# Optimization experiments

Measured on AMD Instinct MI355X. Metric: run time of the kernel, lower is better.

The kernel has to match this reference:

```python
import jax, jax.numpy as jnp
import numpy as np

B, L, V, H = 2, 2048, 1024, 16
HD = V // H  # head size 64
EPS = 1e-3   # keras LayerNormalization default


def setup_inputs() -> dict:
    key = jax.random.key(0)
    ks = jax.random.split(key, 10)
    scale = 1.0 / np.sqrt(V)
    return {
        "query": jax.random.normal(ks[0], (B, L, V), jnp.float32),
        "key_t": jax.random.normal(ks[1], (B, L, V), jnp.float32),
        "value": jax.random.normal(ks[2], (B, L, V), jnp.float32),
        "Wq": jax.random.normal(ks[3], (H, V, HD), jnp.float32) * scale,
        "Wk": jax.random.normal(ks[4], (H, V, HD), jnp.float32) * scale,
        "Wv": jax.random.normal(ks[5], (H, V, HD), jnp.float32) * scale,
        "gamma": jnp.ones((V,), jnp.float32),
        "beta": jnp.zeros((V,), jnp.float32),
        "query_mask": jax.random.randint(ks[6], (B, L), 0, 2, jnp.int32),
        "value_mask": jax.random.randint(ks[7], (B, L), 0, 2, jnp.int32),
    }


def reference(query, key_t, value, Wq, Wk, Wv, gamma, beta, query_mask, value_mask):
    qm = query_mask.astype(jnp.float32)  # (B,L)
    vm = value_mask.astype(jnp.float32)  # (B,L)

    # per-head no-bias Dense projections, batched over heads
    Q = jnp.einsum('blv,hvd->bhld', query, Wq)
    K = jnp.einsum('blv,hvd->bhld', key_t, Wk)
    Vh = jnp.einsum('blv,hvd->bhld', value, Wv)

    scores = jnp.einsum('bhld,bhmd->bhlm', Q, K) / jnp.sqrt(jnp.float32(HD))
    attn = jax.nn.softmax(scores, axis=-1)

    # post-softmax multiplicative masking (faithful to original)
    tri = jnp.tril(jnp.ones((L, L), jnp.float32))  # (L,L) causal
    attn = attn * tri[None, None, :, :]
    attn = attn * qm[:, None, :, None] * vm[:, None, None, :]

    heads = jnp.einsum('bhlm,bhmd->bhld', attn, Vh)
    x = heads.transpose(0, 2, 1, 3).reshape(B, L, V)  # concat heads

    # dropout is identity at inference
    y = x + query
    mu = jnp.mean(y, axis=-1, keepdims=True)
    var = jnp.mean((y - mu) ** 2, axis=-1, keepdims=True)
    return gamma * (y - mu) * jax.lax.rsqrt(var + EPS) + beta
```

## Files before the change

kernel.cpp:

```cpp
#include <hip/hip_runtime.h>
#include <math.h>

constexpr int NB = 2;
constexpr int SL = 2048;
constexpr int NV = 1024;
constexpr int NH = 16;
constexpr int DH = 64;
constexpr float LN_EPS = 1e-3f;

typedef __bf16 bf16_t;
typedef __bf16 v8bf __attribute__((ext_vector_type(8)));
typedef float  v4f  __attribute__((ext_vector_type(4)));

__device__ __forceinline__ unsigned pack_bf16(float a, float b) {
  unsigned short ua = __builtin_bit_cast(unsigned short, (bf16_t)a);
  unsigned short ub = __builtin_bit_cast(unsigned short, (bf16_t)b);
  return (unsigned)ua | ((unsigned)ub << 16);
}
__device__ __forceinline__ void async_cp16(const void* g, void* l) {
  __builtin_amdgcn_global_load_lds(
      (const __attribute__((address_space(1))) unsigned int*)g,
      (__attribute__((address_space(3))) unsigned int*)l, 16, 0, 0);
}

__global__ __launch_bounds__(256)
void wcvt(const float* __restrict__ Wq, const float* __restrict__ Wk,
          const float* __restrict__ Wv, bf16_t* __restrict__ Wt) {
  __shared__ float ls[64][65];
  const int z = blockIdx.z;
  const float* W = z == 0 ? Wq : (z == 1 ? Wk : Wv);
  const float sc = z == 0 ? 0.125f * 1.44269504f : 1.0f;
  const int h = blockIdx.y, v0 = blockIdx.x * 64;
  const int t = threadIdx.x;
  const int rr = t >> 4, c4 = t & 15;
  const float* src = W + ((size_t)h * NV + v0) * DH;
#pragma unroll
  for (int it = 0; it < 4; ++it) {
    float4 f = *(const float4*)(src + (size_t)(rr + it * 16) * DH + c4 * 4);
    ls[rr + it * 16][c4 * 4 + 0] = f.x;
    ls[rr + it * 16][c4 * 4 + 1] = f.y;
    ls[rr + it * 16][c4 * 4 + 2] = f.z;
    ls[rr + it * 16][c4 * 4 + 3] = f.w;
  }
  __syncthreads();
  const int dd = t >> 2, vq = t & 3;
  bf16_t tmp[16];
#pragma unroll
  for (int i = 0; i < 16; ++i) tmp[i] = (bf16_t)(ls[vq * 16 + i][dd] * sc);
  bf16_t* dst = Wt + ((size_t)z * NV + h * 64 + dd) * NV + v0 + vq * 16;
  *(v8bf*)dst = *(v8bf*)&tmp[0];
  *(v8bf*)(dst + 8) = *(v8bf*)&tmp[8];
}

__global__ __launch_bounds__(256, 3)
void proj_mfma(const float* __restrict__ A0, const float* __restrict__ A1,
               const float* __restrict__ A2, const bf16_t* __restrict__ Wtb,
               const int* __restrict__ vmask,
               bf16_t* __restrict__ O0, bf16_t* __restrict__ O1,
               bf16_t* __restrict__ O2) {
  __shared__ __align__(16) bf16_t Asb[2][128 * 40];
  __shared__ __align__(16) bf16_t Wsb[2][128 * 32];

  const int id = blockIdx.x;
  const int z = id >> 8;
  const int m0 = (id & 31) * 128;
  const int n0 = ((id >> 5) & 7) * 128;
  const float*  A   = z == 0 ? A0 : (z == 1 ? A1 : A2);
  bf16_t*       out = z == 0 ? O0 : (z == 1 ? O1 : O2);
  const bf16_t* W   = Wtb + (size_t)z * NV * NV;

  const int t = threadIdx.x, w = t >> 6, lane = t & 63;
  const int g = lane >> 4, lx = lane & 15;
  const int rbase = (w >> 1) * 64, cbase = (w & 1) * 64;

  const int ar_r = t >> 1;
  const int ar_h = (t & 1) * 16;
  float4 ar[4];
  auto gloadA = [&](int k0) {
#pragma unroll
    for (int s = 0; s < 4; ++s)
      ar[s] = *(const float4*)(A + (size_t)(m0 + ar_r) * NV + k0 + ar_h + s * 4);
  };
  auto writeA = [&](int buf) {
    const int c0 = (ar_h >> 3);
    uint4 u0 = {pack_bf16(ar[0].x, ar[0].y), pack_bf16(ar[0].z, ar[0].w),
                pack_bf16(ar[1].x, ar[1].y), pack_bf16(ar[1].z, ar[1].w)};
    uint4 u1 = {pack_bf16(ar[2].x, ar[2].y), pack_bf16(ar[2].z, ar[2].w),
                pack_bf16(ar[3].x, ar[3].y), pack_bf16(ar[3].z, ar[3].w)};
    *(uint4*)((char*)Asb[buf] + ar_r * 80 + (c0 + 0) * 16) = u0;
    *(uint4*)((char*)Asb[buf] + ar_r * 80 + (c0 + 1) * 16) = u1;
  };
  auto stageW = [&](int k0, int buf) {
#pragma unroll
    for (int s = 0; s < 2; ++s) {
      const int r = w * 32 + s * 16 + (lane >> 2);
      const int c = (lane & 3) ^ (r & 3);
      async_cp16(W + (size_t)(n0 + r) * NV + k0 + c * 8,
                 (char*)Wsb[buf] + (w * 32 + s * 16) * 64);
    }
  };

  v4f acc[4][4] = {};

  gloadA(0);
  stageW(0, 0);
  writeA(0);
  __syncthreads();

  for (int it = 0; it < 32; ++it) {
    const int buf = it & 1;
    if (it < 31) { gloadA((it + 1) * 32); stageW((it + 1) * 32, buf ^ 1); }
    v8bf af[4], wf[4];
#pragma unroll
    for (int rt = 0; rt < 4; ++rt) {
      const int row = rbase + rt * 16 + lx;
      af[rt] = *(const v8bf*)((const char*)Asb[buf] + row * 80 + g * 16);
    }
#pragma unroll
    for (int ct = 0; ct < 4; ++ct) {
      const int row = cbase + ct * 16 + lx;
      wf[ct] = *(const v8bf*)((const char*)Wsb[buf] + row * 64 +
                              ((g ^ (row & 3)) * 16));
    }
#pragma unroll
    for (int rt = 0; rt < 4; ++rt)
#pragma unroll
      for (int ct = 0; ct < 4; ++ct)
        acc[rt][ct] = __builtin_amdgcn_mfma_f32_16x16x32_bf16(
            af[rt], wf[ct], acc[rt][ct], 0, 0, 0);
    if (it < 31) { writeA(buf ^ 1); __syncthreads(); }
  }

  if (z < 2) {
#pragma unroll
    for (int rt = 0; rt < 4; ++rt) {
#pragma unroll
      for (int reg = 0; reg < 4; ++reg) {
        const int row = m0 + rbase + rt * 16 + g * 4 + reg;
        const int b = row >> 11, l = row & (SL - 1);
#pragma unroll
        for (int ct = 0; ct < 4; ++ct) {
          const int n = n0 + cbase + ct * 16 + lx;
          const int h = n >> 6, d = n & 63;
          out[((size_t)(b * NH + h) * SL + l) * DH + d] = (bf16_t)acc[rt][ct][reg];
        }
      }
    }
  } else {
#pragma unroll
    for (int rt = 0; rt < 4; ++rt) {
      const int row = m0 + rbase + rt * 16 + g * 4;
      const int b = row >> 11, l = row & (SL - 1);
      float vm0 = (float)vmask[b * SL + l + 0];
      float vm1 = (float)vmask[b * SL + l + 1];
      float vm2 = (float)vmask[b * SL + l + 2];
      float vm3 = (float)vmask[b * SL + l + 3];
#pragma unroll
      for (int ct = 0; ct < 4; ++ct) {
        const int n = n0 + cbase + ct * 16 + lx;
        const int h = n >> 6, d = n & 63;
        uint2 u = {pack_bf16(acc[rt][ct][0] * vm0, acc[rt][ct][1] * vm1),
                   pack_bf16(acc[rt][ct][2] * vm2, acc[rt][ct][3] * vm3)};
        *(uint2*)&out[((size_t)(b * NH + h) * DH + d) * SL + l] = u;
      }
    }
  }
}

__global__ __launch_bounds__(256, 3)
void attn_mfma(const bf16_t* __restrict__ Qg, const bf16_t* __restrict__ Kg,
               const bf16_t* __restrict__ Vtg_all, const int* __restrict__ qmask,
               float* __restrict__ Xout) {
  __shared__ __align__(16) bf16_t kbuf[2][64 * 64];
  __shared__ __align__(16) bf16_t vbuf[2][64 * 64];
  __shared__ __align__(16) bf16_t Ps[4][32][72];

  const int id = blockIdx.x;
  const int bh = (id & 7) | ((id >> 7) << 3);
  const int qb = 15 - ((id >> 3) & 15);
  const int t = threadIdx.x, w = t >> 6, lane = t & 63;
  const int g = lane >> 4, lx = lane & 15;
  const int b = bh >> 4, h = bh & 15;
  const int l0 = qb * 128;
  const int lastAct = 2 * qb + 1;

  const bf16_t* Kb  = Kg + (size_t)bh * SL * DH;
  const bf16_t* Vtg = Vtg_all + (size_t)bh * DH * SL;

  v8bf qf[2][2];
#pragma unroll
  for (int qt = 0; qt < 2; ++qt)
#pragma unroll
    for (int ks = 0; ks < 2; ++ks)
      qf[qt][ks] = *(const v8bf*)&Qg[((size_t)bh * SL + l0 + w * 32 + qt * 16 + lx) * DH +
                                     ks * 32 + g * 8];

  v4f O[2][4] = {};
  float suml[2] = {0.f, 0.f};

  const int sr_off = lane >> 3, sc_l = lane & 7;
  auto stageK = [&](int mb, int buf) {
#pragma unroll
    for (int s = 0; s < 2; ++s) {
      const int r = w * 16 + s * 8 + sr_off;
      const int c = sc_l ^ (r & 7);
      async_cp16(Kb + (size_t)(mb + r) * DH + c * 8,
                 (char*)kbuf[buf] + (w * 16 + s * 8) * 128);
    }
  };
  auto stageV = [&](int mb, int buf) {
#pragma unroll
    for (int s = 0; s < 2; ++s) {
      const int r = w * 16 + s * 8 + sr_off;
      const int c = sc_l ^ (r & 7);
      async_cp16(Vtg + (size_t)r * SL + mb + c * 8,
                 (char*)vbuf[buf] + (w * 16 + s * 8) * 128);
    }
  };

  stageK(0, 0);
  stageV(0, 0);

  for (int mt = 0; mt <= lastAct; ++mt) {
    const int pb = mt & 1;
    __syncthreads();
    if (mt < SL / 64 - 1)  stageK((mt + 1) * 64, pb ^ 1);
    if (mt + 1 <= lastAct) stageV((mt + 1) * 64, pb ^ 1);

    v4f S[4][2];
#pragma unroll
    for (int mt2 = 0; mt2 < 4; ++mt2) {
      S[mt2][0] = (v4f){0.f, 0.f, 0.f, 0.f};
      S[mt2][1] = (v4f){0.f, 0.f, 0.f, 0.f};
    }
#pragma unroll
    for (int ks = 0; ks < 2; ++ks)
#pragma unroll
      for (int mt2 = 0; mt2 < 4; ++mt2) {
        const int row = mt2 * 16 + lx;
        v8bf kf = *(const v8bf*)((const char*)kbuf[pb] + row * 128 +
                                 (((ks * 4 + g) ^ (lx & 7)) * 16));
#pragma unroll
        for (int qt = 0; qt < 2; ++qt)
          S[mt2][qt] = __builtin_amdgcn_mfma_f32_16x16x32_bf16(
              kf, qf[qt][ks], S[mt2][qt], 0, 0, 0);
      }

    const bool diagzone = (mt >= 2 * qb);
#pragma unroll
    for (int mt2 = 0; mt2 < 4; ++mt2)
#pragma unroll
      for (int qt = 0; qt < 2; ++qt) {
        float e0 = __builtin_amdgcn_exp2f(S[mt2][qt][0]);
        float e1 = __builtin_amdgcn_exp2f(S[mt2][qt][1]);
        float e2 = __builtin_amdgcn_exp2f(S[mt2][qt][2]);
        float e3 = __builtin_amdgcn_exp2f(S[mt2][qt][3]);
        suml[qt] += (e0 + e1) + (e2 + e3);
        if (diagzone) {
          const int ml = mt * 64 + mt2 * 16 + g * 4;
          const int ql = l0 + w * 32 + qt * 16 + lx;
          e0 = (ml + 0 <= ql) ? e0 : 0.f;
          e1 = (ml + 1 <= ql) ? e1 : 0.f;
          e2 = (ml + 2 <= ql) ? e2 : 0.f;
          e3 = (ml + 3 <= ql) ? e3 : 0.f;
        }
        uint2 u = {pack_bf16(e0, e1), pack_bf16(e2, e3)};
        *(uint2*)&Ps[w][qt * 16 + lx][mt2 * 16 + g * 4] = u;
      }

#pragma unroll
    for (int ks = 0; ks < 2; ++ks) {
      v8bf pf[2];
#pragma unroll
      for (int qt = 0; qt < 2; ++qt)
        pf[qt] = *(const v8bf*)&Ps[w][qt * 16 + lx][ks * 32 + g * 8];
#pragma unroll
      for (int dt = 0; dt < 4; ++dt) {
        const int row = dt * 16 + lx;
        v8bf vf = *(const v8bf*)((const char*)vbuf[pb] + row * 128 +
                                 (((ks * 4 + g) ^ (lx & 7)) * 16));
#pragma unroll
        for (int qt = 0; qt < 2; ++qt)
          O[qt][dt] = __builtin_amdgcn_mfma_f32_16x16x32_bf16(
              pf[qt], vf, O[qt][dt], 0, 0, 0);
      }
    }
  }

  for (int mt = lastAct + 1; mt < SL / 64; ++mt) {
    const int pb = mt & 1;
    __syncthreads();
    if (mt < SL / 64 - 1) stageK((mt + 1) * 64, pb ^ 1);
    v4f S[4][2];
#pragma unroll
    for (int mt2 = 0; mt2 < 4; ++mt2) {
      S[mt2][0] = (v4f){0.f, 0.f, 0.f, 0.f};
      S[mt2][1] = (v4f){0.f, 0.f, 0.f, 0.f};
    }
#pragma unroll
    for (int ks = 0; ks < 2; ++ks)
#pragma unroll
      for (int mt2 = 0; mt2 < 4; ++mt2) {
        const int row = mt2 * 16 + lx;
        v8bf kf = *(const v8bf*)((const char*)kbuf[pb] + row * 128 +
                                 (((ks * 4 + g) ^ (lx & 7)) * 16));
#pragma unroll
        for (int qt = 0; qt < 2; ++qt)
          S[mt2][qt] = __builtin_amdgcn_mfma_f32_16x16x32_bf16(
              kf, qf[qt][ks], S[mt2][qt], 0, 0, 0);
      }
#pragma unroll
    for (int mt2 = 0; mt2 < 4; ++mt2)
#pragma unroll
      for (int qt = 0; qt < 2; ++qt)
        suml[qt] += (__builtin_amdgcn_exp2f(S[mt2][qt][0]) +
                     __builtin_amdgcn_exp2f(S[mt2][qt][1])) +
                    (__builtin_amdgcn_exp2f(S[mt2][qt][2]) +
                     __builtin_amdgcn_exp2f(S[mt2][qt][3]));
  }

  suml[0] += __shfl_xor(suml[0], 16); suml[0] += __shfl_xor(suml[0], 32);
  suml[1] += __shfl_xor(suml[1], 16); suml[1] += __shfl_xor(suml[1], 32);
#pragma unroll
  for (int qt = 0; qt < 2; ++qt) {
#pragma unroll
    for (int reg = 0; reg < 4; ++reg) {
      const int q = l0 + w * 32 + qt * 16 + g * 4 + reg;
      const float den = __shfl(suml[qt], g * 4 + reg);
      const float inv = (float)qmask[b * SL + q] / den;
#pragma unroll
      for (int dt = 0; dt < 4; ++dt)
        Xout[((size_t)(b * SL + q)) * NV + h * DH + dt * 16 + lx] =
            O[qt][dt][reg] * inv;
    }
  }
}

__global__ __launch_bounds__(256)
void ln_kernel(const float* __restrict__ X, const float* __restrict__ query,
               const float* __restrict__ gamma, const float* __restrict__ beta,
               float* __restrict__ out) {
  const int row0 = blockIdx.x * 2;
  const int t = threadIdx.x;
  float4 gv = *(const float4*)(gamma + t * 4);
  float4 bv = *(const float4*)(beta + t * 4);
  float y[2][4];
  float s[2], ss[2];
#pragma unroll
  for (int r = 0; r < 2; ++r) {
    float4 xv = *(const float4*)(X + (size_t)(row0 + r) * NV + t * 4);
    float4 qv = *(const float4*)(query + (size_t)(row0 + r) * NV + t * 4);
    y[r][0] = xv.x + qv.x; y[r][1] = xv.y + qv.y;
    y[r][2] = xv.z + qv.z; y[r][3] = xv.w + qv.w;
    s[r]  = (y[r][0] + y[r][1]) + (y[r][2] + y[r][3]);
    ss[r] = (y[r][0]*y[r][0] + y[r][1]*y[r][1]) + (y[r][2]*y[r][2] + y[r][3]*y[r][3]);
  }
#pragma unroll
  for (int off = 1; off < 64; off <<= 1) {
    s[0]  += __shfl_xor(s[0], off);  ss[0] += __shfl_xor(ss[0], off);
    s[1]  += __shfl_xor(s[1], off);  ss[1] += __shfl_xor(ss[1], off);
  }
  __shared__ float wsum[2][2][4];
  const int wid = t >> 6;
  if ((t & 63) == 0) {
    wsum[0][0][wid] = s[0]; wsum[0][1][wid] = ss[0];
    wsum[1][0][wid] = s[1]; wsum[1][1][wid] = ss[1];
  }
  __syncthreads();
#pragma unroll
  for (int r = 0; r < 2; ++r) {
    float sr  = (wsum[r][0][0] + wsum[r][0][1]) + (wsum[r][0][2] + wsum[r][0][3]);
    float ssr = (wsum[r][1][0] + wsum[r][1][1]) + (wsum[r][1][2] + wsum[r][1][3]);
    const float mu   = sr * (1.f / NV);
    const float var  = ssr * (1.f / NV) - mu * mu;
    const float rstd = rsqrtf(var + LN_EPS);
    float4 o;
    o.x = gv.x * (y[r][0] - mu) * rstd + bv.x;
    o.y = gv.y * (y[r][1] - mu) * rstd + bv.y;
    o.z = gv.z * (y[r][2] - mu) * rstd + bv.z;
    o.w = gv.w * (y[r][3] - mu) * rstd + bv.w;
    *(float4*)(out + (size_t)(row0 + r) * NV + t * 4) = o;
  }
}

extern "C" void kernel_launch(void* const* d_in, const int* in_sizes, int n_in,
                              void* d_out, int out_size, void* d_ws, size_t ws_size,
                              hipStream_t stream) {
  const float* query = (const float*)d_in[0];
  const float* key_t = (const float*)d_in[1];
  const float* value = (const float*)d_in[2];
  const float* Wq    = (const float*)d_in[3];
  const float* Wk    = (const float*)d_in[4];
  const float* Wv    = (const float*)d_in[5];
  const float* gamma = (const float*)d_in[6];
  const float* beta  = (const float*)d_in[7];
  const int*   qmask = (const int*)d_in[8];
  const int*   vmask = (const int*)d_in[9];
  float* out = (float*)d_out;

  const size_t per = (size_t)NB * NH * SL * DH;
  bf16_t* Qws = (bf16_t*)d_ws;
  bf16_t* Kws = Qws + per;
  bf16_t* Vws = Kws + per;
  bf16_t* Wtb = Vws + per;

  wcvt<<<dim3(16, 16, 3), 256, 0, stream>>>(Wq, Wk, Wv, Wtb);
  proj_mfma<<<768, 256, 0, stream>>>(query, key_t, value, Wtb,
                                     vmask, Qws, Kws, Vws);
  attn_mfma<<<512, 256, 0, stream>>>(Qws, Kws, Vws, qmask, out);
  ln_kernel<<<NB * SL / 2, 256, 0, stream>>>(out, query, gamma, beta, out);
}
```

Measured before the change: 226.8 us.

## Stage fp32 activations asynchronously into LDS and halve projection tile rows

The projection GEMM now copies fp32 activation tiles straight from global memory into swizzled LDS using async global_load_lds, instead of loading them into registers, converting to bf16 and writing them back. The bf16 conversion moves to LDS read time. The M tile shrinks from 128 to 64 rows, so the grid doubles to 1536 blocks and launch bounds target 5 blocks per SIMD. This removes register staging and frees registers for occupancy, but uses more LDS bandwidth for fp32 tiles, adds conversion work in the inner loop, and reloads the W tile twice as often.

```diff
diff --git a/kernel.cpp b/kernel.cpp
--- a/kernel.cpp
+++ b/kernel.cpp
@@ -12,6 +12,12 @@
 typedef __bf16 v8bf __attribute__((ext_vector_type(8)));
 typedef float  v4f  __attribute__((ext_vector_type(4)));
 
+__device__ __forceinline__ v8bf cvt8(float4 a, float4 b) {
+  v8bf v;
+  v[0] = (bf16_t)a.x; v[1] = (bf16_t)a.y; v[2] = (bf16_t)a.z; v[3] = (bf16_t)a.w;
+  v[4] = (bf16_t)b.x; v[5] = (bf16_t)b.y; v[6] = (bf16_t)b.z; v[7] = (bf16_t)b.w;
+  return v;
+}
 __device__ __forceinline__ unsigned pack_bf16(float a, float b) {
   unsigned short ua = __builtin_bit_cast(unsigned short, (bf16_t)a);
   unsigned short ub = __builtin_bit_cast(unsigned short, (bf16_t)b);
@@ -52,43 +58,35 @@
   *(v8bf*)(dst + 8) = *(v8bf*)&tmp[8];
 }
 
-__global__ __launch_bounds__(256, 3)
+__global__ __launch_bounds__(256, 5)
 void proj_mfma(const float* __restrict__ A0, const float* __restrict__ A1,
                const float* __restrict__ A2, const bf16_t* __restrict__ Wtb,
                const int* __restrict__ vmask,
                bf16_t* __restrict__ O0, bf16_t* __restrict__ O1,
                bf16_t* __restrict__ O2) {
-  __shared__ __align__(16) bf16_t Asb[2][128 * 40];
+  __shared__ __align__(16) float  Asb[2][64 * 32];
   __shared__ __align__(16) bf16_t Wsb[2][128 * 32];
 
   const int id = blockIdx.x;
-  const int z = id >> 8;
-  const int m0 = (id & 31) * 128;
-  const int n0 = ((id >> 5) & 7) * 128;
+  const int z  = id >> 9;
+  const int n0 = ((id >> 6) & 7) * 128;
+  const int m0 = (id & 63) * 64;
   const float*  A   = z == 0 ? A0 : (z == 1 ? A1 : A2);
   bf16_t*       out = z == 0 ? O0 : (z == 1 ? O1 : O2);
   const bf16_t* W   = Wtb + (size_t)z * NV * NV;
 
   const int t = threadIdx.x, w = t >> 6, lane = t & 63;
   const int g = lane >> 4, lx = lane & 15;
-  const int rbase = (w >> 1) * 64, cbase = (w & 1) * 64;
-
-  const int ar_r = t >> 1;
-  const int ar_h = (t & 1) * 16;
-  float4 ar[4];
-  auto gloadA = [&](int k0) {
-#pragma unroll
-    for (int s = 0; s < 4; ++s)
-      ar[s] = *(const float4*)(A + (size_t)(m0 + ar_r) * NV + k0 + ar_h + s * 4);
-  };
-  auto writeA = [&](int buf) {
-    const int c0 = (ar_h >> 3);
-    uint4 u0 = {pack_bf16(ar[0].x, ar[0].y), pack_bf16(ar[0].z, ar[0].w),
-                pack_bf16(ar[1].x, ar[1].y), pack_bf16(ar[1].z, ar[1].w)};
-    uint4 u1 = {pack_bf16(ar[2].x, ar[2].y), pack_bf16(ar[2].z, ar[2].w),
-                pack_bf16(ar[3].x, ar[3].y), pack_bf16(ar[3].z, ar[3].w)};
-    *(uint4*)((char*)Asb[buf] + ar_r * 80 + (c0 + 0) * 16) = u0;
-    *(uint4*)((char*)Asb[buf] + ar_r * 80 + (c0 + 1) * 16) = u1;
+  const int rbase = (w >> 1) * 32, cbase = (w & 1) * 64;
+
+  auto stageA = [&](int k0, int buf) {
+#pragma unroll
+    for (int s = 0; s < 2; ++s) {
+      const int r = w * 16 + s * 8 + (lane >> 3);
+      const int c = (lane & 7) ^ (r & 7);
+      async_cp16(A + (size_t)(m0 + r) * NV + k0 + c * 4,
+                 (char*)Asb[buf] + (w * 16 + s * 8) * 128);
+    }
   };
   auto stageW = [&](int k0, int buf) {
 #pragma unroll
@@ -100,21 +98,23 @@
     }
   };
 
-  v4f acc[4][4] = {};
-
-  gloadA(0);
+  v4f acc[2][4] = {};
+
+  stageA(0, 0);
   stageW(0, 0);
-  writeA(0);
   __syncthreads();
 
   for (int it = 0; it < 32; ++it) {
     const int buf = it & 1;
-    if (it < 31) { gloadA((it + 1) * 32); stageW((it + 1) * 32, buf ^ 1); }
-    v8bf af[4], wf[4];
-#pragma unroll
-    for (int rt = 0; rt < 4; ++rt) {
+    if (it < 31) { stageA((it + 1) * 32, buf ^ 1); stageW((it + 1) * 32, buf ^ 1); }
+    v8bf af[2], wf[4];
+#pragma unroll
+    for (int rt = 0; rt < 2; ++rt) {
       const int row = rbase + rt * 16 + lx;
-      af[rt] = *(const v8bf*)((const char*)Asb[buf] + row * 80 + g * 16);
+      const int sw = row & 7;
+      float4 f0 = *(const float4*)((const char*)Asb[buf] + row * 128 + (((2 * g)     ^ sw) * 16));
+      float4 f1 = *(const float4*)((const char*)Asb[buf] + row * 128 + (((2 * g + 1) ^ sw) * 16));
+      af[rt] = cvt8(f0, f1);
     }
 #pragma unroll
     for (int ct = 0; ct < 4; ++ct) {
@@ -123,17 +123,17 @@
                               ((g ^ (row & 3)) * 16));
     }
 #pragma unroll
-    for (int rt = 0; rt < 4; ++rt)
+    for (int rt = 0; rt < 2; ++rt)
 #pragma unroll
       for (int ct = 0; ct < 4; ++ct)
         acc[rt][ct] = __builtin_amdgcn_mfma_f32_16x16x32_bf16(
             af[rt], wf[ct], acc[rt][ct], 0, 0, 0);
-    if (it < 31) { writeA(buf ^ 1); __syncthreads(); }
+    __syncthreads();
   }
 
   if (z < 2) {
 #pragma unroll
-    for (int rt = 0; rt < 4; ++rt) {
+    for (int rt = 0; rt < 2; ++rt) {
 #pragma unroll
       for (int reg = 0; reg < 4; ++reg) {
         const int row = m0 + rbase + rt * 16 + g * 4 + reg;
@@ -148,7 +148,7 @@
     }
   } else {
 #pragma unroll
-    for (int rt = 0; rt < 4; ++rt) {
+    for (int rt = 0; rt < 2; ++rt) {
       const int row = m0 + rbase + rt * 16 + g * 4;
       const int b = row >> 11, l = row & (SL - 1);
       float vm0 = (float)vmask[b * SL + l + 0];
@@ -405,8 +405,8 @@
   bf16_t* Wtb = Vws + per;
 
   wcvt<<<dim3(16, 16, 3), 256, 0, stream>>>(Wq, Wk, Wv, Wtb);
-  proj_mfma<<<768, 256, 0, stream>>>(query, key_t, value, Wtb,
-                                     vmask, Qws, Kws, Vws);
+  proj_mfma<<<1536, 256, 0, stream>>>(query, key_t, value, Wtb,
+                                      vmask, Qws, Kws, Vws);
   attn_mfma<<<512, 256, 0, stream>>>(Qws, Kws, Vws, qmask, out);
   ln_kernel<<<NB * SL / 2, 256, 0, stream>>>(out, query, gamma, beta, out);
 }
```

Result: slower. 234.5 us (+3.4%).
